# Performance work log

Measured on AMD Instinct MI355X. Metric: run time of the kernel, lower is better.

Reference implementation:

```python
import jax, jax.numpy as jnp
import numpy as np

B, S, E, H, G = 2, 2048, 2048, 16, 4
D = E // H  # head dim = 128


def setup_inputs() -> dict:
    key = jax.random.key(0)
    ks = jax.random.split(key, 7)
    scale = 1.0 / np.sqrt(E)
    x = jax.random.normal(ks[0], (B, S, E), dtype=jnp.float32)
    Wq = jax.random.normal(ks[1], (H, E, D), dtype=jnp.float32) * scale
    bq = jax.random.normal(ks[2], (H, D), dtype=jnp.float32) * 0.02
    Wk = jax.random.normal(ks[3], (G, E, D), dtype=jnp.float32) * scale
    bk = jax.random.normal(ks[4], (G, D), dtype=jnp.float32) * 0.02
    Wv = jax.random.normal(ks[5], (G, E, D), dtype=jnp.float32) * scale
    bv = jax.random.normal(ks[6], (G, D), dtype=jnp.float32) * 0.02
    return {"x": x, "Wq": Wq, "bq": bq, "Wk": Wk, "bk": bk, "Wv": Wv, "bv": bv}


def reference(x, Wq, bq, Wk, bk, Wv, bv):
    # x: [B,S,E]; Wq: [H,E,D]; Wk/Wv: [G,E,D]
    h, e, d = Wq.shape
    g = Wk.shape[0]
    per = h // g  # Q heads per KV group
    s = x.shape[1]

    # batched QKV projections (replaces per-head nn.Linear loop)
    q = jnp.einsum('bse,hed->bhsd', x, Wq) + bq[None, :, None, :]   # [B,H,S,D]
    kg = jnp.einsum('bse,ged->bgsd', x, Wk) + bk[None, :, None, :]  # [B,G,S,D]
    vg = jnp.einsum('bse,ged->bgsd', x, Wv) + bv[None, :, None, :]

    # GQA: each KV group serves `per` consecutive Q heads (order i*per+j)
    k = jnp.repeat(kg, per, axis=1)  # [B,H,S,D]
    v = jnp.repeat(vg, per, axis=1)

    scores = jnp.einsum('bhqd,bhkd->bhqk', q, k) * (1.0 / np.sqrt(d))
    causal = jnp.triu(jnp.ones((s, s), dtype=bool), k=1)  # strict upper = masked
    scores = jnp.where(causal[None, None, :, :], -jnp.inf, scores)
    attn = jax.nn.softmax(scores, axis=-1)
    out = jnp.einsum('bhqk,bhkd->bhqd', attn, v)  # [B,H,S,D]
    # concat per-head outputs along feature dim (head order matches loop order)
    return out.transpose(0, 2, 1, 3).reshape(x.shape[0], s, h * d)
```

## Files before the change

kernel.cpp:

```cpp
#include <hip/hip_runtime.h>
#include <hip/hip_bf16.h>
#include <math.h>


typedef __attribute__((ext_vector_type(8))) short bf16x8;
typedef __attribute__((ext_vector_type(4))) short s16x4;
typedef __attribute__((ext_vector_type(4))) float f32x4;

union v8u { bf16x8 v8; s16x4 half[2]; };

#define LOG2E 1.4426950408889634f

__device__ __forceinline__ short f2bf(float f) {
  union { float f; unsigned u; } v; v.f = f;
  unsigned r = v.u + 0x7FFFu + ((v.u >> 16) & 1u);
  return (short)(r >> 16);
}

__device__ __forceinline__ short hwbf(float f) {
  __hip_bfloat16 h = __float2bfloat16(f);
  return *(short*)&h;
}

__device__ __forceinline__ void async16(const void* g, void* l) {
  __builtin_amdgcn_global_load_lds(
      (const __attribute__((address_space(1))) void*)g,
      (__attribute__((address_space(3))) void*)l, 16, 0, 0);
}

__device__ __forceinline__ f32x4 mfma16(bf16x8 a, bf16x8 b, f32x4 c) {
  return __builtin_amdgcn_mfma_f32_16x16x32_bf16(a, b, c, 0, 0, 0);
}


__global__ void conv_x(const float4* __restrict__ x, s16x4* __restrict__ xb) {
  const int i = blockIdx.x * 256 + threadIdx.x;
  float4 v = x[i];
  s16x4 o;
  o[0] = f2bf(v.x); o[1] = f2bf(v.y); o[2] = f2bf(v.z); o[3] = f2bf(v.w);
  xb[i] = o;
}

__global__ void transpose_w(const float* __restrict__ src, short* __restrict__ wt, int c0) {
  __shared__ float t[32][33];
  const int hh = blockIdx.z;
  const int e0 = blockIdx.x * 32, d0 = blockIdx.y * 32;
  const int tx = threadIdx.x, ty = threadIdx.y;
  const float* s = src + (size_t)hh * 2048 * 128;
#pragma unroll
  for (int i = ty; i < 32; i += 8)
    t[i][tx] = s[(size_t)(e0 + i) * 128 + d0 + tx];
  __syncthreads();
#pragma unroll
  for (int i = ty; i < 32; i += 8)
    wt[(size_t)(c0 + hh * 128 + d0 + i) * 2048 + e0 + tx] = f2bf(t[tx][i]);
}

__global__ void build_bias(const float* __restrict__ bq, const float* __restrict__ bk,
                           const float* __restrict__ bv, float* __restrict__ bc) {
  const int c = blockIdx.x * 256 + threadIdx.x;
  float v;
  if (c < 2048)      v = bq[c];
  else if (c < 2560) v = bk[c - 2048];
  else               v = bv[c - 2560];
  bc[c] = v;
}


__global__ __launch_bounds__(256) void qkv_gemm(
    const short* __restrict__ xb, const short* __restrict__ wt,
    const float* __restrict__ bc,
    short* __restrict__ qb, short* __restrict__ kb, short* __restrict__ vt)
{
  constexpr int E = 2048, BK = 32;
  __shared__ short Al[2][128 * BK];
  __shared__ short Bl[2][128 * BK];
  const int tid = threadIdx.x;
  const int lane = tid & 63, wave = tid >> 6;
  const int wr = wave >> 1, wc = wave & 1;
  const int l16 = lane & 15, grp = lane >> 4;
  const int work = (blockIdx.x & 7) * 96 + (blockIdx.x >> 3);
  const int m0 = (work / 24) * 128, n0 = (work % 24) * 128;

  const int c1 = tid, c2 = tid + 256;
  const int r1 = c1 >> 2, s1 = c1 & 3, r2 = c2 >> 2, s2 = c2 & 3;

  f32x4 acc[4][4] = {};

  async16(xb + (size_t)(m0 + r1) * E + s1 * 8, (char*)Al[0] + c1 * 16);
  async16(xb + (size_t)(m0 + r2) * E + s2 * 8, (char*)Al[0] + c2 * 16);
  async16(wt + (size_t)(n0 + r1) * E + s1 * 8, (char*)Bl[0] + c1 * 16);
  async16(wt + (size_t)(n0 + r2) * E + s2 * 8, (char*)Bl[0] + c2 * 16);
  __syncthreads();

  const int nk = E / BK;
  for (int t = 0; t < nk; ++t) {
    const int cur = t & 1;
    if (t + 1 < nk) {
      const int k0 = (t + 1) * BK;
      async16(xb + (size_t)(m0 + r1) * E + k0 + s1 * 8, (char*)Al[cur ^ 1] + c1 * 16);
      async16(xb + (size_t)(m0 + r2) * E + k0 + s2 * 8, (char*)Al[cur ^ 1] + c2 * 16);
      async16(wt + (size_t)(n0 + r1) * E + k0 + s1 * 8, (char*)Bl[cur ^ 1] + c1 * 16);
      async16(wt + (size_t)(n0 + r2) * E + k0 + s2 * 8, (char*)Bl[cur ^ 1] + c2 * 16);
    }
    bf16x8 af[4], bfr[4];
#pragma unroll
    for (int mi = 0; mi < 4; ++mi)
      af[mi] = *(const bf16x8*)&Al[cur][(wr * 64 + mi * 16 + l16) * BK + grp * 8];
#pragma unroll
    for (int ni = 0; ni < 4; ++ni)
      bfr[ni] = *(const bf16x8*)&Bl[cur][(wc * 64 + ni * 16 + l16) * BK + grp * 8];
#pragma unroll
    for (int mi = 0; mi < 4; ++mi)
#pragma unroll
      for (int ni = 0; ni < 4; ++ni)
        acc[mi][ni] = mfma16(af[mi], bfr[ni], acc[mi][ni]);
    __syncthreads();
  }

  const float qscale = 0.08838834764831845f;
#pragma unroll
  for (int ni = 0; ni < 4; ++ni) {
    const int c = n0 + wc * 64 + ni * 16 + l16;
    const float bias = bc[c];
    const int d = c & 127;
#pragma unroll
    for (int mi = 0; mi < 4; ++mi) {
      const int rbase = m0 + wr * 64 + mi * 16 + grp * 4;
      const int b = rbase >> 11;
      const int s = rbase & 2047;
      f32x4 a = acc[mi][ni];
      if (c < 2048) {
        const int h = c >> 7;
        short* dst = qb + ((size_t)(b * 16 + h) * 2048 + s) * 128 + d;
#pragma unroll
        for (int r = 0; r < 4; ++r) dst[(size_t)r * 128] = f2bf((a[r] + bias) * qscale);
      } else if (c < 2560) {
        const int gi = (c >> 7) & 3;
        short* dst = kb + ((size_t)(b * 4 + gi) * 2048 + s) * 128 + d;
#pragma unroll
        for (int r = 0; r < 4; ++r) dst[(size_t)r * 128] = f2bf(a[r] + bias);
      } else {
        const int gi = (c >> 7) & 3;
        s16x4 pk;
#pragma unroll
        for (int r = 0; r < 4; ++r) pk[r] = f2bf(a[r] + bias);
        *(s16x4*)&vt[((size_t)(b * 4 + gi) * 128 + d) * 2048 + s] = pk;
      }
    }
  }
}


__device__ __forceinline__ void stageKV(char* kd, char* vd,
                                        const short* __restrict__ Kg,
                                        const short* __restrict__ Vg,
                                        int kv0, int tid) {
#pragma unroll
  for (int rd = 0; rd < 4; ++rd) {
    const int off = rd * 4096 + tid * 16;
    const int row = off >> 8, colb = off & 255;
    const int sc = colb ^ ((row & 7) << 4);
    async16(Kg + (size_t)(kv0 + row) * 128 + (sc >> 1), kd + off);
  }
#pragma unroll
  for (int rd = 0; rd < 4; ++rd) {
    const int off = rd * 4096 + tid * 16;
    const int row = off >> 7, colb = off & 127;
    const int sc = colb ^ ((row & 7) << 4);
    async16(Vg + (size_t)row * 2048 + kv0 + (sc >> 1), vd + off);
  }
}

__global__ __launch_bounds__(256) void attn(
    const short* __restrict__ qb, const short* __restrict__ kb,
    const short* __restrict__ vt, float* __restrict__ out)
{
  constexpr int S = 2048, D = 128;
  extern __shared__ char lds[];
  const int tid = threadIdx.x;
  const int lane = tid & 63, wave = tid >> 6;
  const int l16 = lane & 15, grp = lane >> 4;
  const int work = (blockIdx.x & 7) * 64 + (blockIdx.x >> 3);
  const int bg = work >> 6, s6 = work & 63;
  const int b = bg >> 2, g = bg & 3;
  const int h = g * 4 + (s6 >> 4);
  const int x = s6 & 15;

  const short* Qg = qb + (size_t)(b * 16 + h) * S * D;
  const short* Kg = kb + (size_t)(b * 4 + g) * S * D;
  const short* Vg = vt + (size_t)(b * 4 + g) * (size_t)D * S;
  const int swz = (l16 & 7) << 4;

#pragma unroll
  for (int p = 0; p < 2; ++p) {
    const int jj = p ? (31 - x) : x;
    const int q0 = jj * 64 + wave * 16;
    const int nt = jj + 1;

    bf16x8 qf[4];
#pragma unroll
    for (int c = 0; c < 4; ++c)
      qf[c] = *(const bf16x8*)&Qg[(size_t)(q0 + l16) * D + c * 32 + grp * 8];

    f32x4 o[8] = {};
    float mrun = -INFINITY, lrun = 0.f;

    stageKV(lds, lds + 32768, Kg, Vg, 0, tid);
    __syncthreads();

    for (int t = 0; t < nt; ++t) {
      const int kv0 = t << 6;
      const int cur = t & 1;
      if (t + 1 < nt)
        stageKV(lds + (cur ^ 1) * 16384, lds + 32768 + (cur ^ 1) * 16384,
                Kg, Vg, kv0 + 64, tid);
      char* const Kb = lds + cur * 16384;
      char* const Vb = lds + 32768 + cur * 16384;

      f32x4 st[4] = {};
      __builtin_amdgcn_s_setprio(1);
#pragma unroll
      for (int c = 0; c < 4; ++c)
#pragma unroll
        for (int f = 0; f < 4; ++f) {
          const int row = f * 16 + l16;
          bf16x8 kf = *(const bf16x8*)(Kb + row * 256 + ((c * 64 + grp * 16) ^ swz));
          st[f] = mfma16(kf, qf[c], st[f]);
        }
      __builtin_amdgcn_s_setprio(0);
      if (t == nt - 1) {
        const int qa = q0 + l16;
#pragma unroll
        for (int f = 0; f < 4; ++f)
#pragma unroll
          for (int r = 0; r < 4; ++r)
            if (kv0 + f * 16 + grp * 4 + r > qa) st[f][r] = -INFINITY;
      }
      float tmax = -INFINITY;
#pragma unroll
      for (int f = 0; f < 4; ++f)
#pragma unroll
        for (int r = 0; r < 4; ++r) tmax = fmaxf(tmax, st[f][r]);
      tmax = fmaxf(tmax, __shfl_xor(tmax, 16));
      tmax = fmaxf(tmax, __shfl_xor(tmax, 32));
      float fac = 1.0f;
      if (!__all(tmax <= mrun + 8.0f)) {
        const float mn = fmaxf(mrun, tmax);
        fac = exp2f((mrun - mn) * LOG2E);
#pragma unroll
        for (int f8 = 0; f8 < 8; ++f8) o[f8] *= fac;
        mrun = mn;
      }
      float lsum = 0.f;
      float ps[16];
#pragma unroll
      for (int f = 0; f < 4; ++f)
#pragma unroll
        for (int r = 0; r < 4; ++r) {
          const float pv = exp2f((st[f][r] - mrun) * LOG2E);
          ps[f * 4 + r] = pv;
          lsum += pv;
        }
      lsum += __shfl_xor(lsum, 16);
      lsum += __shfl_xor(lsum, 32);
      lrun = lrun * fac + lsum;

      bf16x8 pba, pbb;
#pragma unroll
      for (int i = 0; i < 8; ++i) { pba[i] = hwbf(ps[i]); pbb[i] = hwbf(ps[8 + i]); }

      __builtin_amdgcn_s_setprio(1);
#pragma unroll
      for (int f8 = 0; f8 < 8; ++f8) {
        const char* vrow = Vb + (f8 * 16 + l16) * 128;
        v8u va, vb2;
        va.half[0]  = *(const s16x4*)(vrow + ((grp * 8) ^ swz));
        va.half[1]  = *(const s16x4*)(vrow + ((32 + grp * 8) ^ swz));
        o[f8] = mfma16(va.v8, pba, o[f8]);
        vb2.half[0] = *(const s16x4*)(vrow + ((64 + grp * 8) ^ swz));
        vb2.half[1] = *(const s16x4*)(vrow + ((96 + grp * 8) ^ swz));
        o[f8] = mfma16(vb2.v8, pbb, o[f8]);
      }
      __builtin_amdgcn_s_setprio(0);
      __syncthreads();
    }

    const float inv = 1.f / lrun;
    float* orow = out + ((size_t)b * S + q0 + l16) * 2048 + h * D;
#pragma unroll
    for (int f8 = 0; f8 < 8; ++f8) {
      f32x4 v = o[f8] * inv;
      *(f32x4*)&orow[f8 * 16 + grp * 4] = v;
    }
  }
}


extern "C" void kernel_launch(void* const* d_in, const int* in_sizes, int n_in,
                              void* d_out, int out_size, void* d_ws, size_t ws_size,
                              hipStream_t stream) {
  const float* x  = (const float*)d_in[0];
  const float* Wq = (const float*)d_in[1];
  const float* bq = (const float*)d_in[2];
  const float* Wk = (const float*)d_in[3];
  const float* bk = (const float*)d_in[4];
  const float* Wv = (const float*)d_in[5];
  const float* bv = (const float*)d_in[6];
  float* out = (float*)d_out;

  char* ws = (char*)d_ws;
  short* xb = (short*)ws;
  short* wt = (short*)(ws + (size_t)16 * 1024 * 1024);
  float* bc = (float*)(ws + (size_t)28 * 1024 * 1024);
  short* qb = (short*)(ws + (size_t)28 * 1024 * 1024 + 65536);
  short* kb = (short*)((char*)qb + (size_t)16 * 1024 * 1024);
  short* vt = (short*)((char*)kb + (size_t)4 * 1024 * 1024);

  conv_x<<<8192, 256, 0, stream>>>((const float4*)x, (s16x4*)xb);
  dim3 tb(32, 8);
  transpose_w<<<dim3(64, 4, 16), tb, 0, stream>>>(Wq, wt, 0);
  transpose_w<<<dim3(64, 4, 4),  tb, 0, stream>>>(Wk, wt, 2048);
  transpose_w<<<dim3(64, 4, 4),  tb, 0, stream>>>(Wv, wt, 2560);
  build_bias<<<12, 256, 0, stream>>>(bq, bk, bv, bc);
  qkv_gemm<<<768, 256, 0, stream>>>(xb, wt, bc, qb, kb, vt);

  (void)hipFuncSetAttribute((const void*)attn, hipFuncAttributeMaxDynamicSharedMemorySize, 65536);
  attn<<<512, 256, 65536, stream>>>(qb, kb, vt, out);
}
```

Baseline: 264.5 us.

## Switch attention to 32x32x16 MFMA with 128-row query tiles per block

The attention kernel moves from 16x16x32 MFMA to 32x32x16 MFMA. Each wave now owns 32 query rows and each block a 128-row query tile, so the grid halves to 256 blocks. The V-transpose column order is permuted in the QKV GEMM epilogue to match the new P-fragment layout, and the K swizzle widens to 16 rows. Tiles lying entirely above the diagonal are skipped per wave. The aim is to cut LDS reads per FLOP and per-tile softmax overhead, at the cost of more registers per wave and fewer blocks, which leaves only one block per CU on 256 CUs and a less balanced causal workload.

```diff
diff --git a/kernel.cpp b/kernel.cpp
--- a/kernel.cpp
+++ b/kernel.cpp
@@ -6,8 +6,7 @@
 typedef __attribute__((ext_vector_type(8))) short bf16x8;
 typedef __attribute__((ext_vector_type(4))) short s16x4;
 typedef __attribute__((ext_vector_type(4))) float f32x4;
-
-union v8u { bf16x8 v8; s16x4 half[2]; };
+typedef __attribute__((ext_vector_type(16))) float f32x16;
 
 #define LOG2E 1.4426950408889634f
 
@@ -22,6 +21,10 @@
   return *(short*)&h;
 }
 
+__device__ __forceinline__ unsigned pkbf(float a, float b) {
+  return (unsigned)(unsigned short)hwbf(a) | ((unsigned)(unsigned short)hwbf(b) << 16);
+}
+
 __device__ __forceinline__ void async16(const void* g, void* l) {
   __builtin_amdgcn_global_load_lds(
       (const __attribute__((address_space(1))) void*)g,
@@ -30,6 +33,10 @@
 
 __device__ __forceinline__ f32x4 mfma16(bf16x8 a, bf16x8 b, f32x4 c) {
   return __builtin_amdgcn_mfma_f32_16x16x32_bf16(a, b, c, 0, 0, 0);
+}
+
+__device__ __forceinline__ f32x16 mfma32(bf16x8 a, bf16x8 b, f32x16 c) {
+  return __builtin_amdgcn_mfma_f32_32x32x16_bf16(a, b, c, 0, 0, 0);
 }
 
 
@@ -145,7 +152,8 @@
         s16x4 pk;
 #pragma unroll
         for (int r = 0; r < 4; ++r) pk[r] = f2bf(a[r] + bias);
-        *(s16x4*)&vt[((size_t)(b * 4 + gi) * 128 + d) * 2048 + s] = pk;
+        const int vcol = (s & ~12) | ((s & 4) << 1) | ((s & 8) >> 1);
+        *(s16x4*)&vt[((size_t)(b * 4 + gi) * 128 + d) * 2048 + vcol] = pk;
       }
     }
   }
@@ -160,7 +168,7 @@
   for (int rd = 0; rd < 4; ++rd) {
     const int off = rd * 4096 + tid * 16;
     const int row = off >> 8, colb = off & 255;
-    const int sc = colb ^ ((row & 7) << 4);
+    const int sc = colb ^ ((row & 15) << 4);
     async16(Kg + (size_t)(kv0 + row) * 128 + (sc >> 1), kd + off);
   }
 #pragma unroll
@@ -180,30 +188,32 @@
   extern __shared__ char lds[];
   const int tid = threadIdx.x;
   const int lane = tid & 63, wave = tid >> 6;
-  const int l16 = lane & 15, grp = lane >> 4;
-  const int work = (blockIdx.x & 7) * 64 + (blockIdx.x >> 3);
-  const int bg = work >> 6, s6 = work & 63;
+  const int l32 = lane & 31;
+  const int hhf = lane >> 5;
+  const int swzK = (l32 & 15) << 4;
+  const int swzV = (l32 & 7) << 4;
+  const int work = (blockIdx.x & 7) * 32 + (blockIdx.x >> 3);
+  const int bg = work >> 5;
   const int b = bg >> 2, g = bg & 3;
-  const int h = g * 4 + (s6 >> 4);
-  const int x = s6 & 15;
+  const int h = g * 4 + ((work >> 3) & 3);
+  const int x = work & 7;
 
   const short* Qg = qb + (size_t)(b * 16 + h) * S * D;
   const short* Kg = kb + (size_t)(b * 4 + g) * S * D;
   const short* Vg = vt + (size_t)(b * 4 + g) * (size_t)D * S;
-  const int swz = (l16 & 7) << 4;
 
 #pragma unroll
   for (int p = 0; p < 2; ++p) {
-    const int jj = p ? (31 - x) : x;
-    const int q0 = jj * 64 + wave * 16;
-    const int nt = jj + 1;
-
-    bf16x8 qf[4];
-#pragma unroll
-    for (int c = 0; c < 4; ++c)
-      qf[c] = *(const bf16x8*)&Qg[(size_t)(q0 + l16) * D + c * 32 + grp * 8];
-
-    f32x4 o[8] = {};
+    const int jj = p ? (15 - x) : x;
+    const int q0 = jj * 128 + wave * 32;
+    const int nt = 2 * (jj + 1);
+
+    bf16x8 qf[8];
+#pragma unroll
+    for (int c = 0; c < 8; ++c)
+      qf[c] = *(const bf16x8*)&Qg[(size_t)(q0 + l32) * D + c * 16 + hhf * 8];
+
+    f32x16 o[4] = {};
     float mrun = -INFINITY, lrun = 0.f;
 
     stageKV(lds, lds + 32768, Kg, Vg, 0, tid);
@@ -215,84 +225,104 @@
       if (t + 1 < nt)
         stageKV(lds + (cur ^ 1) * 16384, lds + 32768 + (cur ^ 1) * 16384,
                 Kg, Vg, kv0 + 64, tid);
-      char* const Kb = lds + cur * 16384;
-      char* const Vb = lds + 32768 + cur * 16384;
-
-      f32x4 st[4] = {};
-      __builtin_amdgcn_s_setprio(1);
-#pragma unroll
-      for (int c = 0; c < 4; ++c)
-#pragma unroll
-        for (int f = 0; f < 4; ++f) {
-          const int row = f * 16 + l16;
-          bf16x8 kf = *(const bf16x8*)(Kb + row * 256 + ((c * 64 + grp * 16) ^ swz));
-          st[f] = mfma16(kf, qf[c], st[f]);
-        }
-      __builtin_amdgcn_s_setprio(0);
-      if (t == nt - 1) {
-        const int qa = q0 + l16;
-#pragma unroll
-        for (int f = 0; f < 4; ++f)
-#pragma unroll
-          for (int r = 0; r < 4; ++r)
-            if (kv0 + f * 16 + grp * 4 + r > qa) st[f][r] = -INFINITY;
+      const char* Kb = lds + cur * 16384;
+      const char* Vb = lds + 32768 + cur * 16384;
+
+      if (kv0 <= q0 + 31) {
+        f32x16 st[2] = {};
+        __builtin_amdgcn_s_setprio(1);
+#pragma unroll
+        for (int c = 0; c < 8; ++c) {
+          const int X = c * 32 + hhf * 16;
+          bf16x8 k0 = *(const bf16x8*)(Kb + (size_t)l32 * 256 + (X ^ swzK));
+          st[0] = mfma32(k0, qf[c], st[0]);
+          bf16x8 k1 = *(const bf16x8*)(Kb + (size_t)(32 + l32) * 256 + (X ^ swzK));
+          st[1] = mfma32(k1, qf[c], st[1]);
+        }
+        __builtin_amdgcn_s_setprio(0);
+
+        if (kv0 + 63 > q0) {
+          const int qa = q0 + l32;
+#pragma unroll
+          for (int r = 0; r < 16; ++r) {
+            const int kl = (r & 3) + 8 * (r >> 2) + 4 * hhf;
+            if (kv0 + kl > qa)      st[0][r] = -INFINITY;
+            if (kv0 + 32 + kl > qa) st[1][r] = -INFINITY;
+          }
+        }
+
+        float tmax = -INFINITY;
+#pragma unroll
+        for (int r = 0; r < 16; ++r) {
+          tmax = fmaxf(tmax, st[0][r]);
+          tmax = fmaxf(tmax, st[1][r]);
+        }
+        tmax = fmaxf(tmax, __shfl_xor(tmax, 32));
+        float fac = 1.0f;
+        if (!__all(tmax <= mrun + 8.0f)) {
+          const float mn = fmaxf(mrun, tmax);
+          fac = exp2f((mrun - mn) * LOG2E);
+#pragma unroll
+          for (int db = 0; db < 4; ++db) o[db] *= fac;
+          mrun = mn;
+        }
+        float lsum = 0.f;
+        float ps0[16], ps1[16];
+#pragma unroll
+        for (int r = 0; r < 16; ++r) {
+          ps0[r] = exp2f((st[0][r] - mrun) * LOG2E); lsum += ps0[r];
+          ps1[r] = exp2f((st[1][r] - mrun) * LOG2E); lsum += ps1[r];
+        }
+        lsum += __shfl_xor(lsum, 32);
+        lrun = lrun * fac + lsum;
+
+        bf16x8 pf[4];
+#pragma unroll
+        for (int kbi = 0; kbi < 4; ++kbi) {
+          union { unsigned u[4]; bf16x8 v; } tu;
+          const int c0 = 8 * (kbi & 1);
+          if (kbi < 2) {
+            tu.u[0] = pkbf(ps0[c0 + 0], ps0[c0 + 1]);
+            tu.u[1] = pkbf(ps0[c0 + 2], ps0[c0 + 3]);
+            tu.u[2] = pkbf(ps0[c0 + 4], ps0[c0 + 5]);
+            tu.u[3] = pkbf(ps0[c0 + 6], ps0[c0 + 7]);
+          } else {
+            tu.u[0] = pkbf(ps1[c0 + 0], ps1[c0 + 1]);
+            tu.u[1] = pkbf(ps1[c0 + 2], ps1[c0 + 3]);
+            tu.u[2] = pkbf(ps1[c0 + 4], ps1[c0 + 5]);
+            tu.u[3] = pkbf(ps1[c0 + 6], ps1[c0 + 7]);
+          }
+          pf[kbi] = tu.v;
+        }
+
+        __builtin_amdgcn_s_setprio(1);
+#pragma unroll
+        for (int kbi = 0; kbi < 4; ++kbi) {
+          const int X = kbi * 32 + hhf * 16;
+#pragma unroll
+          for (int db = 0; db < 4; ++db) {
+            bf16x8 vf = *(const bf16x8*)(Vb + (size_t)(db * 32 + l32) * 128 + (X ^ swzV));
+            o[db] = mfma32(vf, pf[kbi], o[db]);
+          }
+        }
+        __builtin_amdgcn_s_setprio(0);
       }
-      float tmax = -INFINITY;
-#pragma unroll
-      for (int f = 0; f < 4; ++f)
-#pragma unroll
-        for (int r = 0; r < 4; ++r) tmax = fmaxf(tmax, st[f][r]);
-      tmax = fmaxf(tmax, __shfl_xor(tmax, 16));
-      tmax = fmaxf(tmax, __shfl_xor(tmax, 32));
-      float fac = 1.0f;
-      if (!__all(tmax <= mrun + 8.0f)) {
-        const float mn = fmaxf(mrun, tmax);
-        fac = exp2f((mrun - mn) * LOG2E);
-#pragma unroll
-        for (int f8 = 0; f8 < 8; ++f8) o[f8] *= fac;
-        mrun = mn;
-      }
-      float lsum = 0.f;
-      float ps[16];
-#pragma unroll
-      for (int f = 0; f < 4; ++f)
-#pragma unroll
-        for (int r = 0; r < 4; ++r) {
-          const float pv = exp2f((st[f][r] - mrun) * LOG2E);
-          ps[f * 4 + r] = pv;
-          lsum += pv;
-        }
-      lsum += __shfl_xor(lsum, 16);
-      lsum += __shfl_xor(lsum, 32);
-      lrun = lrun * fac + lsum;
-
-      bf16x8 pba, pbb;
-#pragma unroll
-      for (int i = 0; i < 8; ++i) { pba[i] = hwbf(ps[i]); pbb[i] = hwbf(ps[8 + i]); }
-
-      __builtin_amdgcn_s_setprio(1);
-#pragma unroll
-      for (int f8 = 0; f8 < 8; ++f8) {
-        const char* vrow = Vb + (f8 * 16 + l16) * 128;
-        v8u va, vb2;
-        va.half[0]  = *(const s16x4*)(vrow + ((grp * 8) ^ swz));
-        va.half[1]  = *(const s16x4*)(vrow + ((32 + grp * 8) ^ swz));
-        o[f8] = mfma16(va.v8, pba, o[f8]);
-        vb2.half[0] = *(const s16x4*)(vrow + ((64 + grp * 8) ^ swz));
-        vb2.half[1] = *(const s16x4*)(vrow + ((96 + grp * 8) ^ swz));
-        o[f8] = mfma16(vb2.v8, pbb, o[f8]);
-      }
-      __builtin_amdgcn_s_setprio(0);
       __syncthreads();
     }
 
     const float inv = 1.f / lrun;
-    float* orow = out + ((size_t)b * S + q0 + l16) * 2048 + h * D;
-#pragma unroll
-    for (int f8 = 0; f8 < 8; ++f8) {
-      f32x4 v = o[f8] * inv;
-      *(f32x4*)&orow[f8 * 16 + grp * 4] = v;
-    }
+    float* orow = out + ((size_t)b * S + q0 + l32) * 2048 + h * D;
+#pragma unroll
+    for (int db = 0; db < 4; ++db)
+#pragma unroll
+      for (int rq = 0; rq < 4; ++rq) {
+        f32x4 w;
+        w[0] = o[db][4 * rq + 0] * inv;
+        w[1] = o[db][4 * rq + 1] * inv;
+        w[2] = o[db][4 * rq + 2] * inv;
+        w[3] = o[db][4 * rq + 3] * inv;
+        *(f32x4*)&orow[db * 32 + 8 * rq + 4 * hhf] = w;
+      }
   }
 }
 
@@ -326,5 +356,5 @@
   qkv_gemm<<<768, 256, 0, stream>>>(xb, wt, bc, qb, kb, vt);
 
   (void)hipFuncSetAttribute((const void*)attn, hipFuncAttributeMaxDynamicSharedMemorySize, 65536);
-  attn<<<512, 256, 65536, stream>>>(qb, kb, vt, out);
-}
+  attn<<<256, 256, 65536, stream>>>(qb, kb, vt, out);
+}
```

Result: no change. 267.2 us (+1.0%).
